# Performance work log

Measured on AMD Instinct MI355X. Metric: run time of the kernel, lower is better.

The kernel has to match this reference:

```python
import jax, jax.numpy as jnp
import numpy as np

B, L, E, H = 4, 1024, 1024, 16
D = E // H  # head_dim = 64
K = 3       # conv kernel size
PROB = 0.9  # Bernoulli keep probability


def setup_inputs() -> dict:
    key = jax.random.key(0)
    ks = jax.random.split(key, 8)
    query = jax.random.normal(ks[0], (B, L, E), dtype=jnp.float32)
    keys = jax.random.normal(ks[1], (B, L, E), dtype=jnp.float32)
    values = jax.random.normal(ks[2], (B, L, E), dtype=jnp.float32)
    padding_mask = jax.random.randint(ks[3], (B, L), 0, 2, dtype=jnp.int32)
    causal_mask = jax.random.randint(ks[4], (B, L), 0, 2, dtype=jnp.int32)
    bern_mask = jax.random.bernoulli(ks[5], PROB, (B, H, L)).astype(jnp.int32)
    # learned params: grouped conv (one in/out channel per head) and value linear
    conv_w = jax.random.normal(ks[6], (H, 1, K, K), dtype=jnp.float32) * 0.1
    conv_b = jnp.zeros((H,), dtype=jnp.float32)
    Wv = jax.random.normal(ks[7], (D, D), dtype=jnp.float32) / np.sqrt(D)
    return {"query": query, "keys": keys, "values": values,
            "padding_mask": padding_mask, "causal_mask": causal_mask,
            "bern_mask": bern_mask, "conv_w": conv_w, "conv_b": conv_b, "Wv": Wv}


def _split_heads(x):  # [b, l, (h d)] -> [b, h, l, d]
    b, l, _ = x.shape
    return x.reshape(b, l, H, D).transpose(0, 2, 1, 3)


def reference(query, keys, values, padding_mask, causal_mask, bern_mask, conv_w, conv_b, Wv):
    # queries: grouped conv2d over [b, h=channels, l, d], shape-preserving
    q = _split_heads(query)
    q = jax.lax.conv_general_dilated(
        q, conv_w, window_strides=(1, 1), padding=((1, 1), (1, 1)),
        dimension_numbers=("NCHW", "OIHW", "NCHW"), feature_group_count=H)
    q = q + conv_b[None, :, None, None]
    # keys: Bernoulli-masked fill with -inf, softmax over the SEQ dim (dim=-2)
    k = _split_heads(keys)
    k = jnp.where(bern_mask[..., None].astype(bool), k, -jnp.inf)
    k = jax.nn.softmax(k, axis=-2)
    # values: per-head linear (torch Linear: x @ W^T)
    v = jnp.einsum("bhld,ed->bhle", _split_heads(values), Wv)
    # attention
    energy = jnp.einsum("bhqd,bhkd->bhqk", q, k)
    mask = (padding_mask.astype(bool) & causal_mask.astype(bool))  # [b, k]
    energy = jnp.where(mask[:, None, None, :], jnp.float32(-1e20), energy)
    attn = jax.nn.softmax(energy / jnp.sqrt(jnp.float32(E)), axis=-1)
    out = jnp.einsum("bhqk,bhkd->bhqd", attn, v)
    return out.transpose(0, 2, 1, 3).reshape(query.shape[0], query.shape[1], E)
```

## Files before the change

kernel.cpp:

```cpp
#include <hip/hip_runtime.h>
#include <hip/hip_bf16.h>
#include <math.h>

#define BB 4
#define LL 1024
#define EE 1024
#define HH 16
#define DD 64
#define VROWS 80
#define NCH 8
#define CHROWS 128
#define K2C 0.04508422002777998f

typedef __attribute__((ext_vector_type(8))) short short8;
typedef __attribute__((ext_vector_type(4))) float f32x4;
typedef __attribute__((ext_vector_type(4))) int int4v;

static __device__ __forceinline__ unsigned short bfbits(float x) {
    __hip_bfloat16 h = __float2bfloat16(x);
    return *(unsigned short*)&h;
}

#define CVTPK(dst, lo_, hi_) \
    asm("v_cvt_pk_bf16_f32 %0, %1, %2" : "=v"(dst) : "v"(lo_), "v"(hi_))

__global__ __launch_bounds__(256) void prep_kernel(
    const float* __restrict__ query,
    const float* __restrict__ conv_w,
    const float* __restrict__ conv_b,
    const float* __restrict__ values,
    const float* __restrict__ Wv,
    const float* __restrict__ keys,
    const int* __restrict__ bern,
    const int* __restrict__ pad,
    const int* __restrict__ cau,
    __hip_bfloat16* __restrict__ qcb,
    __hip_bfloat16* __restrict__ vt,
    float* __restrict__ pmax,
    float* __restrict__ psum) {
    __shared__ __align__(16) char SM[34304];
    int tid = threadIdx.x;
    int bid = blockIdx.x;

    if (bid < 4096) {
        int d = tid & 63;
        int lr = tid >> 6;
        int l0 = (bid & (LL / 4 - 1)) << 2;
        int bh = bid >> 8;
        int h = bh & (HH - 1);
        int b = bh >> 4;
        int l = l0 + lr;

        const float* w = conv_w + h * 9;
        float acc = conv_b[h];
        const float* qin = query + ((size_t)b * LL) * EE + h * DD;
        #pragma unroll
        for (int i = 0; i < 3; ++i) {
            int li = l + i - 1;
            if (li < 0 || li >= LL) continue;
            #pragma unroll
            for (int j = 0; j < 3; ++j) {
                int dj = d + j - 1;
                if (dj < 0 || dj >= DD) continue;
                acc += w[i * 3 + j] * qin[(size_t)li * EE + dj];
            }
        }
        qcb[((size_t)bh * LL + l) * DD + d] = __float2bfloat16(acc * K2C);
    } else if (bid < 5120) {
        float (*WvS)[65] = (float(*)[65])SM;
        float (*vs)[68]  = (float(*)[68])(SM + 16640);
        float* mS = (float*)(SM + 34048);
        int tile = bid - 4096;
        int lt = tile & 15;
        int bh = tile >> 4;
        int h = bh & (HH - 1);
        int b = bh >> 4;
        int l0 = lt * 64;

        if (tid < 64) {
            int l = l0 + tid;
            mS[tid] = ((pad[b * LL + l] != 0) & (cau[b * LL + l] != 0)) ? 0.f : 1.f;
        }
        for (int idx = tid; idx < 64 * 64; idx += 256)
            WvS[idx >> 6][idx & 63] = Wv[idx];
        const float* vin = values + ((size_t)b * LL + l0) * EE + h * DD;
        for (int idx = tid; idx < 1024; idx += 256) {
            int r = idx >> 4;
            int c4 = (idx & 15) << 2;
            *(float4*)&vs[r][c4] = *(const float4*)&vin[(size_t)r * EE + c4];
        }
        __syncthreads();

        int d = tid & 63;
        int r0 = (tid >> 6) * 16;
        float acc[16];
        #pragma unroll
        for (int r = 0; r < 16; ++r) acc[r] = 0.f;
        for (int k = 0; k < 64; ++k) {
            float wv = WvS[d][k];
            #pragma unroll
            for (int r = 0; r < 16; ++r) acc[r] += vs[r0 + r][k] * wv;
        }
        #pragma unroll
        for (int r = 0; r < 16; ++r) acc[r] *= mS[r0 + r];
        union { unsigned short us[16]; uint2 u2[4]; } pk;
        #pragma unroll
        for (int r = 0; r < 16; ++r) pk.us[r] = bfbits(acc[r]);
        int a = tid >> 6;
        int C32 = (a >> 1) << 5;
        int h4 = a & 1;
        __hip_bfloat16* vo = vt + ((size_t)bh * VROWS + d) * LL + l0 + C32 + 4 * h4;
        #pragma unroll
        for (int g2 = 0; g2 < 4; ++g2)
            *(uint2*)&vo[8 * g2] = pk.u2[g2];

        if (tid < 64) {
            int aa = tid >> 4, g2 = (tid >> 2) & 3, m = tid & 3;
            int dst = l0 + 32 * (aa >> 1) + 4 * (aa & 1) + 8 * g2 + m;
            vt[((size_t)bh * VROWS + 64) * LL + dst] = __float2bfloat16(mS[tid]);
        }
        for (int idx = tid; idx < 15 * 64; idx += 256) {
            int rr = idx >> 6, l = idx & 63;
            vt[((size_t)bh * VROWS + 65 + rr) * LL + l0 + l] = __float2bfloat16(0.f);
        }
    } else {
        float (*sm)[64] = (float(*)[64])SM;
        float (*ss)[64] = (float(*)[64])(SM + 1024);
        int blk = bid - 5120;
        int d = tid & 63;
        int seg = tid >> 6;
        int ch = blk & (NCH - 1);
        int bh = blk >> 3;
        int h = bh & (HH - 1);
        int b = bh >> 4;
        int r0 = ch * CHROWS + seg * 32;

        const float* kin = keys + ((size_t)b * LL + r0) * EE + h * DD + d;
        const int* bm = bern + (size_t)bh * LL + r0;

        float v[32];
        #pragma unroll
        for (int i = 0; i < 32; ++i) v[i] = kin[(size_t)i * EE];
        float m = -INFINITY;
        #pragma unroll
        for (int i = 0; i < 32; ++i)
            if (bm[i]) m = fmaxf(m, v[i]);
        float s = 0.f;
        #pragma unroll
        for (int i = 0; i < 32; ++i)
            if (bm[i]) s += __expf(v[i] - m);

        sm[seg][d] = m;
        ss[seg][d] = s;
        __syncthreads();
        if (seg == 0) {
            float M = sm[0][d];
            #pragma unroll
            for (int t = 1; t < 4; ++t) M = fmaxf(M, sm[t][d]);
            float S = 0.f;
            if (M > -INFINITY) {
                #pragma unroll
                for (int t = 0; t < 4; ++t)
                    if (sm[t][d] > -INFINITY) S += ss[t][d] * __expf(sm[t][d] - M);
            }
            pmax[(size_t)blk * 64 + d] = M;
            psum[(size_t)blk * 64 + d] = S;
        }
    }
}

__global__ __launch_bounds__(256) void ksm_final_kernel(
    const float* __restrict__ keys,
    const int* __restrict__ bern,
    const float* __restrict__ pmax,
    const float* __restrict__ psum,
    __hip_bfloat16* __restrict__ ksb) {
    int tid = threadIdx.x;
    int d = tid & 63;
    int seg = tid >> 6;
    int blk = blockIdx.x;
    int ch = blk & (NCH - 1);
    int bh = blk >> 3;
    int h = bh & (HH - 1);
    int b = bh >> 4;
    int r0 = ch * CHROWS + seg * 32;

    const float* pm = pmax + (size_t)bh * NCH * 64;
    const float* ps = psum + (size_t)bh * NCH * 64;
    float M = -INFINITY;
    #pragma unroll
    for (int c = 0; c < NCH; ++c) M = fmaxf(M, pm[c * 64 + d]);
    float S = 0.f;
    #pragma unroll
    for (int c = 0; c < NCH; ++c) {
        float mi = pm[c * 64 + d];
        if (mi > -INFINITY) S += ps[c * 64 + d] * __expf(mi - M);
    }
    float inv = 1.f / S;

    const float* kin = keys + ((size_t)b * LL + r0) * EE + h * DD + d;
    const int* bm = bern + (size_t)bh * LL + r0;
    __hip_bfloat16* kout = ksb + ((size_t)bh * LL + r0) * DD + d;
    #pragma unroll
    for (int i = 0; i < 32; ++i) {
        float val = bm[i] ? __expf(kin[(size_t)i * EE] - M) * inv : 0.f;
        kout[(size_t)i * DD] = __float2bfloat16(val);
    }
}

__global__ __launch_bounds__(256) void attn_mfma_kernel(
    const __hip_bfloat16* __restrict__ qcb,
    const __hip_bfloat16* __restrict__ ksb,
    const __hip_bfloat16* __restrict__ vtb,
    float* __restrict__ out) {
    __shared__ __align__(16) short KsS[2][4096];
    __shared__ __align__(16) short VtS[2][5120];

    int tid = threadIdx.x;
    int lane = tid & 63;
    int w = tid >> 6;
    int q15 = lane & 15;
    int g = (lane >> 4) & 3;

    int bid = blockIdx.x;
    int swz = (bid & 7) * 128 + (bid >> 3);
    int bh = swz >> 4;
    int qb = swz & 15;
    int b = bh >> 4;
    int h = bh & 15;
    int q0w = qb * 64 + w * 16;

    int srow = tid >> 3;
    int sch = tid & 7;
    int ssw = (sch ^ (srow & 7)) << 3;
    const short* kg = (const short*)ksb + (size_t)bh * LL * DD + (size_t)srow * DD + ssw;
    const short* vg = (const short*)vtb + (size_t)bh * VROWS * LL + (size_t)srow * LL + ssw;
    const short* vgx = (const short*)vtb + (size_t)bh * VROWS * LL + (size_t)(64 + srow) * LL + ssw;

    short8 Qf0, Qf1;
    {
        const short* qrow = (const short*)qcb + ((size_t)bh * LL + q0w + q15) * DD + 8 * g;
        Qf0 = *(const short8*)(qrow);
        Qf1 = *(const short8*)(qrow + 32);
    }

    #pragma unroll
    for (int it = 0; it < 2; ++it) {
        __builtin_amdgcn_global_load_lds(
            (const __attribute__((address_space(1))) void*)(kg + (size_t)(it * 32) * DD),
            (__attribute__((address_space(3))) void*)&KsS[0][(it * 4 + w) * 512], 16, 0, 0);
        __builtin_amdgcn_global_load_lds(
            (const __attribute__((address_space(1))) void*)(vg + (size_t)it * 32 * LL),
            (__attribute__((address_space(3))) void*)&VtS[0][(it * 4 + w) * 512], 16, 0, 0);
    }
    if (w < 2) {
        __builtin_amdgcn_global_load_lds(
            (const __attribute__((address_space(1))) void*)(vgx),
            (__attribute__((address_space(3))) void*)&VtS[0][4096 + w * 512], 16, 0, 0);
    }

    f32x4 O[4], O5;
    #pragma unroll
    for (int u = 0; u < 4; ++u) O[u] = (f32x4){0.f, 0.f, 0.f, 0.f};
    O5 = (f32x4){0.f, 0.f, 0.f, 0.f};

    for (int kt = 0; kt < 16; ++kt) {
        __syncthreads();

        if (kt < 15) {
            int nb = (kt + 1) & 1;
            int k0n = (kt + 1) * 64;
            #pragma unroll
            for (int it = 0; it < 2; ++it) {
                __builtin_amdgcn_global_load_lds(
                    (const __attribute__((address_space(1))) void*)(kg + (size_t)(k0n + it * 32) * DD),
                    (__attribute__((address_space(3))) void*)&KsS[nb][(it * 4 + w) * 512], 16, 0, 0);
                __builtin_amdgcn_global_load_lds(
                    (const __attribute__((address_space(1))) void*)(vg + k0n + (size_t)it * 32 * LL),
                    (__attribute__((address_space(3))) void*)&VtS[nb][(it * 4 + w) * 512], 16, 0, 0);
            }
            if (w < 2) {
                __builtin_amdgcn_global_load_lds(
                    (const __attribute__((address_space(1))) void*)(vgx + k0n),
                    (__attribute__((address_space(3))) void*)&VtS[nb][4096 + w * 512], 16, 0, 0);
            }
        }

        int cb = kt & 1;
        const short* Kb = KsS[cb];
        const short* Vb = VtS[cb];
        int sw = q15 & 7;
        int off0 = (g ^ sw) << 3;
        int off1 = ((g + 4) ^ sw) << 3;

        f32x4 S[4];
        __builtin_amdgcn_s_setprio(1);
        #pragma unroll
        for (int t = 0; t < 4; ++t) {
            short8 kf0 = *(const short8*)&Kb[(16 * t + q15) * 64 + off0];
            short8 kf1 = *(const short8*)&Kb[(16 * t + q15) * 64 + off1];
            f32x4 z = (f32x4){0.f, 0.f, 0.f, 0.f};
            z = __builtin_amdgcn_mfma_f32_16x16x32_bf16(kf0, Qf0, z, 0, 0, 0);
            S[t] = __builtin_amdgcn_mfma_f32_16x16x32_bf16(kf1, Qf1, z, 0, 0, 0);
        }
        __builtin_amdgcn_s_setprio(0);

        short8 vfa[5], vfb[5];
        #pragma unroll
        for (int u = 0; u < 5; ++u) {
            vfa[u] = *(const short8*)&Vb[(16 * u + q15) * 64 + off0];
            vfb[u] = *(const short8*)&Vb[(16 * u + q15) * 64 + off1];
        }

        float pv[4][4];
        #pragma unroll
        for (int t = 0; t < 4; ++t)
            #pragma unroll
            for (int r = 0; r < 4; ++r)
                pv[t][r] = exp2f(S[t][r]);

        int4v pa0, pa1;
        {
            int d0, d1, d2, d3;
            CVTPK(d0, pv[0][0], pv[0][1]);
            CVTPK(d1, pv[0][2], pv[0][3]);
            CVTPK(d2, pv[1][0], pv[1][1]);
            CVTPK(d3, pv[1][2], pv[1][3]);
            pa0 = (int4v){d0, d1, d2, d3};
            CVTPK(d0, pv[2][0], pv[2][1]);
            CVTPK(d1, pv[2][2], pv[2][3]);
            CVTPK(d2, pv[3][0], pv[3][1]);
            CVTPK(d3, pv[3][2], pv[3][3]);
            pa1 = (int4v){d0, d1, d2, d3};
        }
        union PW { int4v i4; short8 s8; } pw0, pw1;
        pw0.i4 = pa0;
        pw1.i4 = pa1;

        __builtin_amdgcn_s_setprio(1);
        #pragma unroll
        for (int u = 0; u < 4; ++u) {
            O[u] = __builtin_amdgcn_mfma_f32_16x16x32_bf16(vfa[u], pw0.s8, O[u], 0, 0, 0);
            O[u] = __builtin_amdgcn_mfma_f32_16x16x32_bf16(vfb[u], pw1.s8, O[u], 0, 0, 0);
        }
        O5 = __builtin_amdgcn_mfma_f32_16x16x32_bf16(vfa[4], pw0.s8, O5, 0, 0, 0);
        O5 = __builtin_amdgcn_mfma_f32_16x16x32_bf16(vfb[4], pw1.s8, O5, 0, 0, 0);
        __builtin_amdgcn_s_setprio(0);
    }

    float ls = __shfl(O5[0], q15, 64);
    float invl = 1.f / ls;

    float* gout = out + ((size_t)b * LL + q0w + q15) * EE + h * DD + 4 * g;
    #pragma unroll
    for (int u = 0; u < 4; ++u) {
        float4 vv = { O[u][0] * invl, O[u][1] * invl, O[u][2] * invl, O[u][3] * invl };
        *(float4*)&gout[16 * u] = vv;
    }
}

extern "C" void kernel_launch(void* const* d_in, const int* in_sizes, int n_in,
                              void* d_out, int out_size, void* d_ws, size_t ws_size,
                              hipStream_t stream) {
    const float* query = (const float*)d_in[0];
    const float* keys  = (const float*)d_in[1];
    const float* values = (const float*)d_in[2];
    const int* pad  = (const int*)d_in[3];
    const int* cau  = (const int*)d_in[4];
    const int* bern = (const int*)d_in[5];
    const float* conv_w = (const float*)d_in[6];
    const float* conv_b = (const float*)d_in[7];
    const float* Wv = (const float*)d_in[8];
    float* outp = (float*)d_out;

    const size_t per = (size_t)BB * HH * LL * DD;
    const size_t vper = (size_t)BB * HH * VROWS * LL;
    __hip_bfloat16* qcb = (__hip_bfloat16*)d_ws;
    __hip_bfloat16* ksb = qcb + per;
    __hip_bfloat16* vtb = ksb + per;
    float* pmax = (float*)(vtb + vper);
    float* psum = pmax + (size_t)BB * HH * NCH * 64;

    prep_kernel<<<5632, 256, 0, stream>>>(query, conv_w, conv_b, values, Wv,
                                          keys, bern, pad, cau,
                                          qcb, vtb, pmax, psum);
    ksm_final_kernel<<<BB * HH * NCH, 256, 0, stream>>>(keys, bern, pmax, psum, ksb);
    attn_mfma_kernel<<<BB * HH * 16, 256, 0, stream>>>(qcb, ksb, vtb, outp);
}
```

Baseline: 74.67 us.

## Process two query sub-tiles per wave to reuse K/V LDS fragments

Each wave now handles 32 query rows (two 16-row sub-tiles) instead of 16, so each block covers 128 queries and the grid is halved. K and V fragments read from LDS are reused across both sub-tiles, halving LDS reads and global K/V staging per query. The cost is more accumulator registers per thread and fewer blocks, 512 instead of 1024, which may reduce occupancy and latency hiding on a device with many CUs.

```diff
diff --git a/kernel.cpp b/kernel.cpp
--- a/kernel.cpp
+++ b/kernel.cpp
@@ -223,12 +223,12 @@
     int g = (lane >> 4) & 3;
 
     int bid = blockIdx.x;
-    int swz = (bid & 7) * 128 + (bid >> 3);
-    int bh = swz >> 4;
-    int qb = swz & 15;
+    int swz = (bid & 7) * 64 + (bid >> 3);
+    int bh = swz >> 3;
+    int qb = swz & 7;
     int b = bh >> 4;
     int h = bh & 15;
-    int q0w = qb * 64 + w * 16;
+    int q0w = qb * 128 + w * 32;
 
     int srow = tid >> 3;
     int sch = tid & 7;
@@ -237,11 +237,12 @@
     const short* vg = (const short*)vtb + (size_t)bh * VROWS * LL + (size_t)srow * LL + ssw;
     const short* vgx = (const short*)vtb + (size_t)bh * VROWS * LL + (size_t)(64 + srow) * LL + ssw;
 
-    short8 Qf0, Qf1;
-    {
-        const short* qrow = (const short*)qcb + ((size_t)bh * LL + q0w + q15) * DD + 8 * g;
-        Qf0 = *(const short8*)(qrow);
-        Qf1 = *(const short8*)(qrow + 32);
+    short8 Qf[2][2];
+    #pragma unroll
+    for (int s = 0; s < 2; ++s) {
+        const short* qrow = (const short*)qcb + ((size_t)bh * LL + q0w + 16 * s + q15) * DD + 8 * g;
+        Qf[s][0] = *(const short8*)(qrow);
+        Qf[s][1] = *(const short8*)(qrow + 32);
     }
 
     #pragma unroll
@@ -259,10 +260,13 @@
             (__attribute__((address_space(3))) void*)&VtS[0][4096 + w * 512], 16, 0, 0);
     }
 
-    f32x4 O[4], O5;
-    #pragma unroll
-    for (int u = 0; u < 4; ++u) O[u] = (f32x4){0.f, 0.f, 0.f, 0.f};
-    O5 = (f32x4){0.f, 0.f, 0.f, 0.f};
+    f32x4 O[2][4], O5[2];
+    #pragma unroll
+    for (int s = 0; s < 2; ++s) {
+        #pragma unroll
+        for (int u = 0; u < 4; ++u) O[s][u] = (f32x4){0.f, 0.f, 0.f, 0.f};
+        O5[s] = (f32x4){0.f, 0.f, 0.f, 0.f};
+    }
 
     for (int kt = 0; kt < 16; ++kt) {
         __syncthreads();
@@ -293,15 +297,23 @@
         int off0 = (g ^ sw) << 3;
         int off1 = ((g + 4) ^ sw) << 3;
 
-        f32x4 S[4];
+        short8 kf0[4], kf1[4];
+        #pragma unroll
+        for (int t = 0; t < 4; ++t) {
+            kf0[t] = *(const short8*)&Kb[(16 * t + q15) * 64 + off0];
+            kf1[t] = *(const short8*)&Kb[(16 * t + q15) * 64 + off1];
+        }
+
+        f32x4 S[2][4];
         __builtin_amdgcn_s_setprio(1);
         #pragma unroll
-        for (int t = 0; t < 4; ++t) {
-            short8 kf0 = *(const short8*)&Kb[(16 * t + q15) * 64 + off0];
-            short8 kf1 = *(const short8*)&Kb[(16 * t + q15) * 64 + off1];
-            f32x4 z = (f32x4){0.f, 0.f, 0.f, 0.f};
-            z = __builtin_amdgcn_mfma_f32_16x16x32_bf16(kf0, Qf0, z, 0, 0, 0);
-            S[t] = __builtin_amdgcn_mfma_f32_16x16x32_bf16(kf1, Qf1, z, 0, 0, 0);
+        for (int s = 0; s < 2; ++s) {
+            #pragma unroll
+            for (int t = 0; t < 4; ++t) {
+                f32x4 z = (f32x4){0.f, 0.f, 0.f, 0.f};
+                z = __builtin_amdgcn_mfma_f32_16x16x32_bf16(kf0[t], Qf[s][0], z, 0, 0, 0);
+                S[s][t] = __builtin_amdgcn_mfma_f32_16x16x32_bf16(kf1[t], Qf[s][1], z, 0, 0, 0);
+            }
         }
         __builtin_amdgcn_s_setprio(0);
 
@@ -312,50 +324,53 @@
             vfb[u] = *(const short8*)&Vb[(16 * u + q15) * 64 + off1];
         }
 
-        float pv[4][4];
-        #pragma unroll
-        for (int t = 0; t < 4; ++t)
-            #pragma unroll
-            for (int r = 0; r < 4; ++r)
-                pv[t][r] = exp2f(S[t][r]);
-
-        int4v pa0, pa1;
-        {
+        union PW { int4v i4; short8 s8; } pw0[2], pw1[2];
+        #pragma unroll
+        for (int s = 0; s < 2; ++s) {
+            float pv[4][4];
+            #pragma unroll
+            for (int t = 0; t < 4; ++t)
+                #pragma unroll
+                for (int r = 0; r < 4; ++r)
+                    pv[t][r] = exp2f(S[s][t][r]);
             int d0, d1, d2, d3;
             CVTPK(d0, pv[0][0], pv[0][1]);
             CVTPK(d1, pv[0][2], pv[0][3]);
             CVTPK(d2, pv[1][0], pv[1][1]);
             CVTPK(d3, pv[1][2], pv[1][3]);
-            pa0 = (int4v){d0, d1, d2, d3};
+            pw0[s].i4 = (int4v){d0, d1, d2, d3};
             CVTPK(d0, pv[2][0], pv[2][1]);
             CVTPK(d1, pv[2][2], pv[2][3]);
             CVTPK(d2, pv[3][0], pv[3][1]);
             CVTPK(d3, pv[3][2], pv[3][3]);
-            pa1 = (int4v){d0, d1, d2, d3};
-        }
-        union PW { int4v i4; short8 s8; } pw0, pw1;
-        pw0.i4 = pa0;
-        pw1.i4 = pa1;
+            pw1[s].i4 = (int4v){d0, d1, d2, d3};
+        }
 
         __builtin_amdgcn_s_setprio(1);
         #pragma unroll
+        for (int s = 0; s < 2; ++s) {
+            #pragma unroll
+            for (int u = 0; u < 4; ++u) {
+                O[s][u] = __builtin_amdgcn_mfma_f32_16x16x32_bf16(vfa[u], pw0[s].s8, O[s][u], 0, 0, 0);
+                O[s][u] = __builtin_amdgcn_mfma_f32_16x16x32_bf16(vfb[u], pw1[s].s8, O[s][u], 0, 0, 0);
+            }
+            O5[s] = __builtin_amdgcn_mfma_f32_16x16x32_bf16(vfa[4], pw0[s].s8, O5[s], 0, 0, 0);
+            O5[s] = __builtin_amdgcn_mfma_f32_16x16x32_bf16(vfb[4], pw1[s].s8, O5[s], 0, 0, 0);
+        }
+        __builtin_amdgcn_s_setprio(0);
+    }
+
+    #pragma unroll
+    for (int s = 0; s < 2; ++s) {
+        float ls = __shfl(O5[s][0], q15, 64);
+        float invl = 1.f / ls;
+        float* gout = out + ((size_t)b * LL + q0w + 16 * s + q15) * EE + h * DD + 4 * g;
+        #pragma unroll
         for (int u = 0; u < 4; ++u) {
-            O[u] = __builtin_amdgcn_mfma_f32_16x16x32_bf16(vfa[u], pw0.s8, O[u], 0, 0, 0);
-            O[u] = __builtin_amdgcn_mfma_f32_16x16x32_bf16(vfb[u], pw1.s8, O[u], 0, 0, 0);
-        }
-        O5 = __builtin_amdgcn_mfma_f32_16x16x32_bf16(vfa[4], pw0.s8, O5, 0, 0, 0);
-        O5 = __builtin_amdgcn_mfma_f32_16x16x32_bf16(vfb[4], pw1.s8, O5, 0, 0, 0);
-        __builtin_amdgcn_s_setprio(0);
-    }
-
-    float ls = __shfl(O5[0], q15, 64);
-    float invl = 1.f / ls;
-
-    float* gout = out + ((size_t)b * LL + q0w + q15) * EE + h * DD + 4 * g;
-    #pragma unroll
-    for (int u = 0; u < 4; ++u) {
-        float4 vv = { O[u][0] * invl, O[u][1] * invl, O[u][2] * invl, O[u][3] * invl };
-        *(float4*)&gout[16 * u] = vv;
+            float4 vv = { O[s][u][0] * invl, O[s][u][1] * invl,
+                          O[s][u][2] * invl, O[s][u][3] * invl };
+            *(float4*)&gout[16 * u] = vv;
+        }
     }
 }
 
@@ -385,5 +400,5 @@
                                           keys, bern, pad, cau,
                                           qcb, vtb, pmax, psum);
     ksm_final_kernel<<<BB * HH * NCH, 256, 0, stream>>>(keys, bern, pmax, psum, ksb);
-    attn_mfma_kernel<<<BB * HH * 16, 256, 0, stream>>>(qcb, ksb, vtb, outp);
+    attn_mfma_kernel<<<BB * HH * 8, 256, 0, stream>>>(qcb, ksb, vtb, outp);
 }
```

New measurement: 75.22 us. About the same (+0.7%).

## Fold key softmax normalization into query and drop max pass over keys

Applied to the files above, without the earlier changes.

Key softmax is computed without max subtraction, so exp(k) is written to bf16 in a single pass over keys while partial sums are accumulated. A tiny kernel turns the sums into per-(head, d) reciprocals, which the attention kernel multiplies into the query fragments. This removes the second read of the keys tensor and the separate normalization kernel. The cost is possible overflow for large key values and an extra bf16 rounding of the scaled query.

```diff
diff --git a/kernel.cpp b/kernel.cpp
--- a/kernel.cpp
+++ b/kernel.cpp
@@ -19,6 +19,10 @@
 static __device__ __forceinline__ unsigned short bfbits(float x) {
     __hip_bfloat16 h = __float2bfloat16(x);
     return *(unsigned short*)&h;
+}
+static __device__ __forceinline__ float bf2f(unsigned short u) {
+    unsigned int x = (unsigned int)u << 16;
+    return *(float*)&x;
 }
 
 #define CVTPK(dst, lo_, hi_) \
@@ -36,7 +40,7 @@
     const int* __restrict__ cau,
     __hip_bfloat16* __restrict__ qcb,
     __hip_bfloat16* __restrict__ vt,
-    float* __restrict__ pmax,
+    __hip_bfloat16* __restrict__ ksb,
     float* __restrict__ psum) {
     __shared__ __align__(16) char SM[34304];
     int tid = threadIdx.x;
@@ -124,8 +128,7 @@
             vt[((size_t)bh * VROWS + 65 + rr) * LL + l0 + l] = __float2bfloat16(0.f);
         }
     } else {
-        float (*sm)[64] = (float(*)[64])SM;
-        float (*ss)[64] = (float(*)[64])(SM + 1024);
+        float (*ss)[64] = (float(*)[64])SM;
         int blk = bid - 5120;
         int d = tid & 63;
         int seg = tid >> 6;
@@ -137,81 +140,42 @@
 
         const float* kin = keys + ((size_t)b * LL + r0) * EE + h * DD + d;
         const int* bm = bern + (size_t)bh * LL + r0;
-
-        float v[32];
-        #pragma unroll
-        for (int i = 0; i < 32; ++i) v[i] = kin[(size_t)i * EE];
-        float m = -INFINITY;
-        #pragma unroll
-        for (int i = 0; i < 32; ++i)
-            if (bm[i]) m = fmaxf(m, v[i]);
+        __hip_bfloat16* kout = ksb + ((size_t)bh * LL + r0) * DD + d;
+
         float s = 0.f;
         #pragma unroll
-        for (int i = 0; i < 32; ++i)
-            if (bm[i]) s += __expf(v[i] - m);
-
-        sm[seg][d] = m;
+        for (int i = 0; i < 32; ++i) {
+            float ek = bm[i] ? __expf(kin[(size_t)i * EE]) : 0.f;
+            s += ek;
+            kout[(size_t)i * DD] = __float2bfloat16(ek);
+        }
         ss[seg][d] = s;
         __syncthreads();
         if (seg == 0) {
-            float M = sm[0][d];
-            #pragma unroll
-            for (int t = 1; t < 4; ++t) M = fmaxf(M, sm[t][d]);
-            float S = 0.f;
-            if (M > -INFINITY) {
-                #pragma unroll
-                for (int t = 0; t < 4; ++t)
-                    if (sm[t][d] > -INFINITY) S += ss[t][d] * __expf(sm[t][d] - M);
-            }
-            pmax[(size_t)blk * 64 + d] = M;
+            float S = (ss[0][d] + ss[1][d]) + (ss[2][d] + ss[3][d]);
             psum[(size_t)blk * 64 + d] = S;
         }
     }
 }
 
-__global__ __launch_bounds__(256) void ksm_final_kernel(
-    const float* __restrict__ keys,
-    const int* __restrict__ bern,
-    const float* __restrict__ pmax,
+__global__ __launch_bounds__(256) void invs_kernel(
     const float* __restrict__ psum,
-    __hip_bfloat16* __restrict__ ksb) {
-    int tid = threadIdx.x;
-    int d = tid & 63;
-    int seg = tid >> 6;
-    int blk = blockIdx.x;
-    int ch = blk & (NCH - 1);
-    int bh = blk >> 3;
-    int h = bh & (HH - 1);
-    int b = bh >> 4;
-    int r0 = ch * CHROWS + seg * 32;
-
-    const float* pm = pmax + (size_t)bh * NCH * 64;
-    const float* ps = psum + (size_t)bh * NCH * 64;
-    float M = -INFINITY;
-    #pragma unroll
-    for (int c = 0; c < NCH; ++c) M = fmaxf(M, pm[c * 64 + d]);
+    float* __restrict__ invS) {
+    int idx = blockIdx.x * 256 + threadIdx.x;
+    int bh = idx >> 6;
+    int d = idx & 63;
+    const float* p = psum + (size_t)bh * NCH * 64 + d;
     float S = 0.f;
     #pragma unroll
-    for (int c = 0; c < NCH; ++c) {
-        float mi = pm[c * 64 + d];
-        if (mi > -INFINITY) S += ps[c * 64 + d] * __expf(mi - M);
-    }
-    float inv = 1.f / S;
-
-    const float* kin = keys + ((size_t)b * LL + r0) * EE + h * DD + d;
-    const int* bm = bern + (size_t)bh * LL + r0;
-    __hip_bfloat16* kout = ksb + ((size_t)bh * LL + r0) * DD + d;
-    #pragma unroll
-    for (int i = 0; i < 32; ++i) {
-        float val = bm[i] ? __expf(kin[(size_t)i * EE] - M) * inv : 0.f;
-        kout[(size_t)i * DD] = __float2bfloat16(val);
-    }
+    for (int c = 0; c < NCH; ++c) S += p[c * 64];
+    invS[idx] = 1.f / S;
 }
 
 __global__ __launch_bounds__(256) void attn_mfma_kernel(
     const __hip_bfloat16* __restrict__ qcb,
     const __hip_bfloat16* __restrict__ ksb,
     const __hip_bfloat16* __restrict__ vtb,
+    const float* __restrict__ invS,
     float* __restrict__ out) {
     __shared__ __align__(16) short KsS[2][4096];
     __shared__ __align__(16) short VtS[2][5120];
@@ -240,8 +204,14 @@
     short8 Qf0, Qf1;
     {
         const short* qrow = (const short*)qcb + ((size_t)bh * LL + q0w + q15) * DD + 8 * g;
-        Qf0 = *(const short8*)(qrow);
-        Qf1 = *(const short8*)(qrow + 32);
+        short8 r0 = *(const short8*)(qrow);
+        short8 r1 = *(const short8*)(qrow + 32);
+        const float* isb = invS + (size_t)bh * 64 + 8 * g;
+        #pragma unroll
+        for (int j = 0; j < 8; ++j) {
+            Qf0[j] = (short)bfbits(bf2f((unsigned short)r0[j]) * isb[j]);
+            Qf1[j] = (short)bfbits(bf2f((unsigned short)r1[j]) * isb[32 + j]);
+        }
     }
 
     #pragma unroll
@@ -378,12 +348,12 @@
     __hip_bfloat16* qcb = (__hip_bfloat16*)d_ws;
     __hip_bfloat16* ksb = qcb + per;
     __hip_bfloat16* vtb = ksb + per;
-    float* pmax = (float*)(vtb + vper);
-    float* psum = pmax + (size_t)BB * HH * NCH * 64;
+    float* psum = (float*)(vtb + vper);
+    float* invS = psum + (size_t)BB * HH * NCH * 64;
 
     prep_kernel<<<5632, 256, 0, stream>>>(query, conv_w, conv_b, values, Wv,
                                           keys, bern, pad, cau,
-                                          qcb, vtb, pmax, psum);
-    ksm_final_kernel<<<BB * HH * NCH, 256, 0, stream>>>(keys, bern, pmax, psum, ksb);
-    attn_mfma_kernel<<<BB * HH * 16, 256, 0, stream>>>(qcb, ksb, vtb, outp);
-}
+                                          qcb, vtb, ksb, psum);
+    invs_kernel<<<16, 256, 0, stream>>>(psum, invS);
+    attn_mfma_kernel<<<BB * HH * 16, 256, 0, stream>>>(qcb, ksb, vtb, invS, outp);
+}
```

After: 76.17 us. +2.0%, slower.
